# Kernel optimization log

Measured on AMD Instinct MI355X. Metric: run time of the kernel, lower is better.

Reference implementation:

```python
import jax, jax.numpy as jnp
import numpy as np

N = 100000
E = 1600000
G = 2048
D = 128
F_IN = 9
BN_EPS = 1e-5


def setup_inputs() -> dict:
    key = jax.random.key(0)
    ks = jax.random.split(key, 20)
    def glorot(k, shape):
        lim = float(np.sqrt(6.0 / (shape[0] + shape[1])))
        return jax.random.uniform(k, shape, jnp.float32, -lim, lim)
    inp = {
        'x': jax.random.normal(ks[0], (N, F_IN), jnp.float32),
        'edge_index': jax.random.randint(ks[1], (2, E), 0, N, jnp.int64),
        'batch_index': jnp.sort(jax.random.randint(ks[2], (N,), 0, G, jnp.int64)),
        'W0': glorot(ks[3], (F_IN, D)), 'b0': jnp.zeros((D,), jnp.float32),
        'W1': glorot(ks[4], (D, D)), 'b1': jnp.zeros((D,), jnp.float32),
        'W2': glorot(ks[5], (D, D)), 'b2': jnp.zeros((D,), jnp.float32),
        'W3': glorot(ks[6], (D, D)), 'b3': jnp.zeros((D,), jnp.float32),
        'g1': jnp.ones((D,), jnp.float32), 'be1': jnp.zeros((D,), jnp.float32),
        'g2': jnp.ones((D,), jnp.float32), 'be2': jnp.zeros((D,), jnp.float32),
        'g3': jnp.ones((D,), jnp.float32), 'be3': jnp.zeros((D,), jnp.float32),
        'Wout': glorot(ks[7], (D, 1)), 'bout': jnp.zeros((1,), jnp.float32),
    }
    return inp


def _gcn_conv(x, W, b, row, col, dinv):
    # PyG GCNConv: out = D^-1/2 (A+I) D^-1/2 (x W) + b
    lin = x @ W                                  # [N, D]
    coef = (dinv[row] * dinv[col])[:, None]      # [E, 1]
    agg = jax.ops.segment_sum(lin[row] * coef, col, num_segments=N)
    agg = agg + (dinv * dinv)[:, None] * lin     # self-loop term
    return agg + b


def _bn(x, gamma, beta):
    # BatchNorm1d training-mode: batch stats over node dim, biased variance
    m = jnp.mean(x, axis=0)
    v = jnp.var(x, axis=0)
    return (x - m) * jax.lax.rsqrt(v + BN_EPS) * gamma + beta


def reference(x, edge_index, batch_index, W0, b0, W1, b1, W2, b2, W3, b3,
              g1, be1, g2, be2, g3, be3, Wout, bout):
    row, col = edge_index[0], edge_index[1]
    # degrees with self-loops (all edge weights = 1)
    deg = jax.ops.segment_sum(jnp.ones((E,), x.dtype), col, num_segments=N) + 1.0
    dinv = jax.lax.rsqrt(deg)
    lrelu = lambda h: jax.nn.leaky_relu(h, negative_slope=0.01)

    h = _bn(lrelu(_gcn_conv(x, W0, b0, row, col, dinv)), g1, be1)
    h = _bn(lrelu(_gcn_conv(h, W1, b1, row, col, dinv)), g2, be2)
    h = _bn(lrelu(_gcn_conv(h, W2, b2, row, col, dinv)), g3, be3)
    h = lrelu(_gcn_conv(h, W3, b3, row, col, dinv))

    # global mean pool over graphs
    sums = jax.ops.segment_sum(h, batch_index, num_segments=G)
    cnts = jax.ops.segment_sum(jnp.ones((N,), x.dtype), batch_index, num_segments=G)
    pooled = sums / jnp.maximum(cnts, 1.0)[:, None]   # [G, D]
    return pooled @ Wout + bout                       # [G, 1]
```

## Files before the change

### kernel.cpp

```cpp
#include <hip/hip_runtime.h>


#define LRELU(z) ((z) > 0.f ? (z) : 0.01f * (z))

typedef __attribute__((ext_vector_type(8))) short short8;
typedef __attribute__((ext_vector_type(4))) float float4v;

__device__ inline unsigned bf16_rn(float a) {
  unsigned u = __float_as_uint(a);
  return (u + 0x7FFFu + ((u >> 16) & 1u)) >> 16;
}

__device__ inline unsigned pack_bf16x2(float a, float b) {
  return bf16_rn(a) | (bf16_rn(b) << 16);
}

__device__ inline float bf16f(unsigned short s) {
  return __uint_as_float(((unsigned)s) << 16);
}

__device__ inline float4 unpack_bf16x4(uint2 u) {
  float4 r;
  r.x = __uint_as_float(u.x << 16);
  r.y = __uint_as_float(u.x & 0xffff0000u);
  r.z = __uint_as_float(u.y << 16);
  r.w = __uint_as_float(u.y & 0xffff0000u);
  return r;
}

__device__ inline void accb(int4& d, unsigned v) {
  d.x += ((int)(v << 24)) >> 24;
  d.y += ((int)(v << 16)) >> 24;
  d.z += ((int)(v << 8)) >> 24;
  d.w += ((int)v) >> 24;
}

__global__ __launch_bounds__(256) void k_count(const int* __restrict__ ei,
                                               int* __restrict__ cnt,
                                               int* __restrict__ rank, int E) {
  int i = blockIdx.x * 256 + threadIdx.x;
  if (i < E) rank[i] = atomicAdd(&cnt[ei[E + i]], 1);
}

__global__ __launch_bounds__(256) void k_scan1(const int* __restrict__ cnt,
                                               int* __restrict__ incl,
                                               int* __restrict__ bsums,
                                               float* __restrict__ dinv, int N) {
  __shared__ int s[256];
  int tid = threadIdx.x;
  int idx = blockIdx.x * 256 + tid;
  int v = (idx < N) ? cnt[idx] : 0;
  if (idx < N) dinv[idx] = rsqrtf((float)(v + 1));
  s[tid] = v;
  __syncthreads();
  for (int off = 1; off < 256; off <<= 1) {
    int t = (tid >= off) ? s[tid - off] : 0;
    __syncthreads();
    s[tid] += t;
    __syncthreads();
  }
  if (idx < N) incl[idx] = s[tid];
  if (tid == 255) bsums[blockIdx.x] = s[255];
}

__global__ __launch_bounds__(512) void k_scan2(const int* __restrict__ bsums,
                                               int* __restrict__ bpref, int nb) {
  __shared__ int s[512];
  int tid = threadIdx.x;
  int v = (tid < nb) ? bsums[tid] : 0;
  s[tid] = v;
  __syncthreads();
  for (int off = 1; off < 512; off <<= 1) {
    int t = (tid >= off) ? s[tid - off] : 0;
    __syncthreads();
    s[tid] += t;
    __syncthreads();
  }
  bpref[tid] = s[tid] - v;
}

__global__ __launch_bounds__(256) void k_cntg(const int* __restrict__ batch,
                                              float* __restrict__ cntG,
                                              int N, int G) {
  int g = blockIdx.x * 256 + threadIdx.x;
  if (g >= G) return;
  int lo = 0, hi = N;
  while (lo < hi) { int mid = (lo + hi) >> 1; if (batch[mid] < g) lo = mid + 1; else hi = mid; }
  int a = lo;
  hi = N;
  while (lo < hi) { int mid = (lo + hi) >> 1; if (batch[mid] < g + 1) lo = mid + 1; else hi = mid; }
  cntG[g] = (float)(lo - a);
}

__global__ __launch_bounds__(256) void k_scan3_prep(
    const int* __restrict__ incl, const int* __restrict__ cnt,
    const int* __restrict__ bpref, int* __restrict__ offs,
    int2* __restrict__ meta, const float* __restrict__ x,
    const float* __restrict__ dinv, unsigned* __restrict__ u, int N) {
  int idx = blockIdx.x * 256 + threadIdx.x;
  if (idx >= N) return;
  int c = cnt[idx];
  int off = incl[idx] - c + bpref[blockIdx.x];
  offs[idx] = off;
  meta[idx] = make_int2(off, c);
  float dv = dinv[idx];
  const float* xr = x + (size_t)idx * 9;
  unsigned p0 = pack_bf16x2(xr[0] * dv, xr[1] * dv);
  unsigned p1 = pack_bf16x2(xr[2] * dv, xr[3] * dv);
  unsigned p2 = pack_bf16x2(xr[4] * dv, xr[5] * dv);
  unsigned p3 = pack_bf16x2(xr[6] * dv, xr[7] * dv);
  unsigned p4 = pack_bf16x2(xr[8] * dv, dv);
  uint2* u2 = (uint2*)u;
  u2[(size_t)idx * 3 + 0] = make_uint2(p0, p1);
  u2[(size_t)idx * 3 + 1] = make_uint2(p2, p3);
  u2[(size_t)idx * 3 + 2] = make_uint2(p4, 0u);
}

__global__ __launch_bounds__(256) void k_csr(const int* __restrict__ ei,
                                             const int* __restrict__ offs,
                                             const int* __restrict__ rank,
                                             int* __restrict__ rows, int E) {
  int i = blockIdx.x * 256 + threadIdx.x;
  if (i < E) {
    int c = ei[E + i];
    rows[offs[c] + rank[i]] = ei[i];
  }
}

__global__ __launch_bounds__(256) void k_spmm9(
    const unsigned short* __restrict__ u, const int2* __restrict__ meta,
    const int* __restrict__ rows, const float* __restrict__ dinv,
    float* __restrict__ ax, float2* __restrict__ dq, int N) {
  const int t = threadIdx.x;
  const int g = t >> 4;
  const int f = t & 15;
  const int v = blockIdx.x * 16 + g;
  if (v >= N) return;
  const int2 m = meta[v];
  const int st = m.x;
  const int dg = m.y;
  const float dv = dinv[v];
  const bool act = (f < 10);
  float a0 = (f < 9) ? bf16f(u[(unsigned)v * 12u + f]) : 0.f;
  float a1 = 0.f, a2 = 0.f, a3 = 0.f;
  int idx = 0;
  if (f < (dg < 16 ? dg : 16)) idx = rows[st + f];
  for (int b = 0; b < dg; b += 16) {
    int rem = dg - b;
    int mm = rem < 16 ? rem : 16;
    const int cur = idx;
    if (b + 16 < dg) idx = (f < rem - 16) ? rows[st + b + 16 + f] : 0;
    int e = 0;
    for (; e + 8 <= mm; e += 8) {
      int r0 = __shfl(cur, e + 0, 16), r1 = __shfl(cur, e + 1, 16);
      int r2 = __shfl(cur, e + 2, 16), r3 = __shfl(cur, e + 3, 16);
      int r4 = __shfl(cur, e + 4, 16), r5 = __shfl(cur, e + 5, 16);
      int r6 = __shfl(cur, e + 6, 16), r7 = __shfl(cur, e + 7, 16);
      float x0 = 0, x1 = 0, x2 = 0, x3 = 0, x4 = 0, x5 = 0, x6 = 0, x7 = 0;
      if (act) {
        x0 = bf16f(u[(unsigned)r0 * 12u + f]); x1 = bf16f(u[(unsigned)r1 * 12u + f]);
        x2 = bf16f(u[(unsigned)r2 * 12u + f]); x3 = bf16f(u[(unsigned)r3 * 12u + f]);
        x4 = bf16f(u[(unsigned)r4 * 12u + f]); x5 = bf16f(u[(unsigned)r5 * 12u + f]);
        x6 = bf16f(u[(unsigned)r6 * 12u + f]); x7 = bf16f(u[(unsigned)r7 * 12u + f]);
      }
      a0 += x0; a1 += x1; a2 += x2; a3 += x3;
      a0 += x4; a1 += x5; a2 += x6; a3 += x7;
    }
    for (; e + 4 <= mm; e += 4) {
      int r0 = __shfl(cur, e + 0, 16), r1 = __shfl(cur, e + 1, 16);
      int r2 = __shfl(cur, e + 2, 16), r3 = __shfl(cur, e + 3, 16);
      float x0 = 0, x1 = 0, x2 = 0, x3 = 0;
      if (act) {
        x0 = bf16f(u[(unsigned)r0 * 12u + f]); x1 = bf16f(u[(unsigned)r1 * 12u + f]);
        x2 = bf16f(u[(unsigned)r2 * 12u + f]); x3 = bf16f(u[(unsigned)r3 * 12u + f]);
      }
      a0 += x0; a1 += x1; a2 += x2; a3 += x3;
    }
    for (; e < mm; e++) {
      int r = __shfl(cur, e, 16);
      if (act) a0 += bf16f(u[(unsigned)r * 12u + f]);
    }
  }
  float sum = (a0 + a1) + (a2 + a3);
  if (f < 9) {
    ax[(unsigned)v * 12u + f] = sum * dv;
  } else if (f == 9) {
    dq[v] = make_float2(dv, dv * (dv + sum));
  }
}

__global__ __launch_bounds__(256) void k_gemm_in(
    const float* __restrict__ ax, const float* __restrict__ W0,
    const float* __restrict__ b0, unsigned short* __restrict__ Abuf,
    float* __restrict__ part, int N) {
  __shared__ float Wl[9 * 128];
  __shared__ float rs[128], rq[128];
  const int t = threadIdx.x;
  for (int i = t; i < 9 * 128; i += 256) Wl[i] = W0[i];
  if (t < 128) { rs[t] = 0.f; rq[t] = 0.f; }
  __syncthreads();
  const int col = t & 127;
  const int rsub = t >> 7;
  const int base = blockIdx.x * 16;
  const float bc = b0[col];
  float ls = 0.f, lq = 0.f;
  for (int it = 0; it < 8; it++) {
    int row = base + it * 2 + rsub;
    if (row < N) {
      const float* ar = ax + (size_t)row * 12;
      float acc = bc;
#pragma unroll
      for (int k = 0; k < 9; k++) acc += ar[k] * Wl[k * 128 + col];
      float a = LRELU(acc);
      Abuf[(size_t)row * 128 + col] = (unsigned short)bf16_rn(a);
      ls += a;
      lq += a * a;
    }
  }
  atomicAdd(&rs[col], ls);
  atomicAdd(&rq[col], lq);
  __syncthreads();
  if (t < 128) {
    float* pr = part + (size_t)blockIdx.x * 256;
    pr[t] = rs[t];
    pr[128 + t] = rq[t];
  }
}

__global__ __launch_bounds__(256) void k_redstats(const float* __restrict__ part,
                                                  float* __restrict__ stats,
                                                  int nrows) {
  const int t = threadIdx.x;
  float s = 0.f;
  for (int r = blockIdx.x; r < nrows; r += gridDim.x)
    s += part[(size_t)r * 256 + t];
  atomicAdd(&stats[t], s);
}

__global__ __launch_bounds__(256) void k_gemm_mfma(
    const unsigned short* __restrict__ Ab, const uint4* __restrict__ Wb,
    const float* __restrict__ dinv, unsigned short* __restrict__ Lb,
    unsigned* __restrict__ colmaxU, int N) {
  __shared__ uint4 Bl[2048];
  __shared__ unsigned short Dl[4 * 2048];
  __shared__ float dvs[64];
  __shared__ unsigned cmx[128];
  const int t = threadIdx.x;
  const int row0 = blockIdx.x * 64;
#pragma unroll
  for (int i = 0; i < 8; i++) Bl[t + i * 256] = Wb[t + i * 256];
  if (t < 128) cmx[t] = 0u;
  if (t < 64) {
    int r = row0 + t;
    dvs[t] = (r < N) ? dinv[r] : 0.f;
  }
  __syncthreads();
  const int w = t >> 6;
  const int lane = t & 63;
  const int m = lane & 15;
  const int quad = lane >> 4;
  const int rowA = min(row0 + w * 16 + m, N - 1);
  const uint4* Arow = (const uint4*)(Ab + (size_t)rowA * 128);
  uint4 a[4];
#pragma unroll
  for (int kt = 0; kt < 4; kt++) a[kt] = Arow[kt * 4 + quad];
  float4v acc[8];
#pragma unroll
  for (int nt = 0; nt < 8; nt++) acc[nt] = (float4v)0.0f;
#pragma unroll
  for (int nt = 0; nt < 8; nt++) {
#pragma unroll
    for (int kt = 0; kt < 4; kt++) {
      uint4 b = Bl[((kt * 8 + nt) * 4 + quad) * 16 + m];
      acc[nt] = __builtin_amdgcn_mfma_f32_16x16x32_bf16(
          *(short8*)&a[kt], *(short8*)&b, acc[nt], 0, 0, 0);
    }
  }
  unsigned short* Dw = Dl + w * 2048;
  float cm8[8];
#pragma unroll
  for (int nt = 0; nt < 8; nt++) cm8[nt] = 0.f;
#pragma unroll
  for (int r = 0; r < 4; r++) {
    float dv = dvs[w * 16 + quad * 4 + r];
#pragma unroll
    for (int nt = 0; nt < 8; nt++) {
      float fv = acc[nt][r] * dv;
      Dw[(quad * 4 + r) * 128 + nt * 16 + m] = (unsigned short)bf16_rn(fv);
      cm8[nt] = fmaxf(cm8[nt], fabsf(fv));
    }
  }
#pragma unroll
  for (int nt = 0; nt < 8; nt++)
    atomicMax(&cmx[nt * 16 + m], __float_as_uint(cm8[nt]));
  __syncthreads();
  const uint4* Dw4 = (const uint4*)Dw;
#pragma unroll
  for (int p = 0; p < 4; p++) {
    int row = row0 + w * 16 + p * 4 + (lane >> 4);
    if (row < N) {
      ((uint4*)(Lb + (size_t)row * 128))[lane & 15] = Dw4[p * 64 + lane];
    }
  }
  if (t < 128) atomicMax(&colmaxU[t], cmx[t]);
}

__global__ __launch_bounds__(256) void k_quant(
    const unsigned short* __restrict__ Lb, const unsigned* __restrict__ cmU,
    unsigned* __restrict__ L8, int N4) {
  __shared__ float invS[128];
  const int t = threadIdx.x;
  if (t < 128) {
    float cm = __uint_as_float(cmU[t]);
    invS[t] = cm > 0.f ? 127.f / cm : 0.f;
  }
  __syncthreads();
  int idx = blockIdx.x * 256 + t;
  if (idx >= N4) return;
  const int row = idx >> 2;
  const int seg = idx & 3;
  const uint2* src = (const uint2*)(Lb + (size_t)row * 128 + seg * 32);
  const float* inv = invS + seg * 32;
  unsigned d[8];
#pragma unroll
  for (int j = 0; j < 8; j++) {
    float4 f = unpack_bf16x4(src[j]);
    int q0 = __float2int_rn(f.x * inv[j * 4 + 0]);
    int q1 = __float2int_rn(f.y * inv[j * 4 + 1]);
    int q2 = __float2int_rn(f.z * inv[j * 4 + 2]);
    int q3 = __float2int_rn(f.w * inv[j * 4 + 3]);
    q0 = max(-127, min(127, q0));
    q1 = max(-127, min(127, q1));
    q2 = max(-127, min(127, q2));
    q3 = max(-127, min(127, q3));
    d[j] = (unsigned)(q0 & 255) | ((unsigned)(q1 & 255) << 8) |
           ((unsigned)(q2 & 255) << 16) | ((unsigned)(q3 & 255) << 24);
  }
  uint4* dst = (uint4*)((char*)L8 + (size_t)row * 128 + (size_t)seg * 32);
  dst[0] = make_uint4(d[0], d[1], d[2], d[3]);
  dst[1] = make_uint4(d[4], d[5], d[6], d[7]);
}

__device__ inline int4 gacci(const unsigned* __restrict__ L8d,
                             const int* __restrict__ rows,
                             int st, int dg, int idx, int q32) {
  int4 s0 = make_int4(0, 0, 0, 0), s1 = s0, s2 = s0, s3 = s0;
  for (int b = 0; b < dg; b += 32) {
    int rem = dg - b;
    int mm = rem < 32 ? rem : 32;
    const int cur = idx;
    if (b + 32 < dg) idx = (q32 < rem - 32) ? rows[st + b + 32 + q32] : 0;
    int e = 0;
    for (; e + 8 <= mm; e += 8) {
      int r0 = __shfl(cur, e + 0, 32), r1 = __shfl(cur, e + 1, 32);
      int r2 = __shfl(cur, e + 2, 32), r3 = __shfl(cur, e + 3, 32);
      int r4 = __shfl(cur, e + 4, 32), r5 = __shfl(cur, e + 5, 32);
      int r6 = __shfl(cur, e + 6, 32), r7 = __shfl(cur, e + 7, 32);
      unsigned w0 = L8d[((unsigned)r0 << 5) + q32];
      unsigned w1 = L8d[((unsigned)r1 << 5) + q32];
      unsigned w2 = L8d[((unsigned)r2 << 5) + q32];
      unsigned w3 = L8d[((unsigned)r3 << 5) + q32];
      unsigned w4 = L8d[((unsigned)r4 << 5) + q32];
      unsigned w5 = L8d[((unsigned)r5 << 5) + q32];
      unsigned w6 = L8d[((unsigned)r6 << 5) + q32];
      unsigned w7 = L8d[((unsigned)r7 << 5) + q32];
      accb(s0, w0); accb(s1, w1); accb(s2, w2); accb(s3, w3);
      accb(s0, w4); accb(s1, w5); accb(s2, w6); accb(s3, w7);
    }
    for (; e + 4 <= mm; e += 4) {
      int r0 = __shfl(cur, e + 0, 32), r1 = __shfl(cur, e + 1, 32);
      int r2 = __shfl(cur, e + 2, 32), r3 = __shfl(cur, e + 3, 32);
      unsigned w0 = L8d[((unsigned)r0 << 5) + q32];
      unsigned w1 = L8d[((unsigned)r1 << 5) + q32];
      unsigned w2 = L8d[((unsigned)r2 << 5) + q32];
      unsigned w3 = L8d[((unsigned)r3 << 5) + q32];
      accb(s0, w0); accb(s1, w1); accb(s2, w2); accb(s3, w3);
    }
    for (; e < mm; e++) {
      int r = __shfl(cur, e, 32);
      unsigned w0 = L8d[((unsigned)r << 5) + q32];
      accb(s0, w0);
    }
  }
  int4 acc;
  acc.x = (s0.x + s1.x) + (s2.x + s3.x);
  acc.y = (s0.y + s1.y) + (s2.y + s3.y);
  acc.z = (s0.z + s1.z) + (s2.z + s3.z);
  acc.w = (s0.w + s1.w) + (s2.w + s3.w);
  return acc;
}

template <int MODE>
__global__ __launch_bounds__(256) void k_spmm(
    const unsigned* __restrict__ Lb, const unsigned* __restrict__ L8d,
    const unsigned* __restrict__ cmU, const int2* __restrict__ meta,
    const int* __restrict__ rows, const float2* __restrict__ dq,
    const float* __restrict__ tw, const float* __restrict__ bias,
    unsigned short* __restrict__ Aout, float* __restrict__ part,
    const float* __restrict__ wout, const int* __restrict__ batch,
    float* __restrict__ pacc, int N) {
  const int t = threadIdx.x;
  const int g = t >> 5;
  const int q32 = t & 31;
  const uint2* __restrict__ L2p = (const uint2*)Lb;
  const float4 t4 = ((const float4*)tw)[q32];
  const float4 b4 = ((const float4*)bias)[q32];
  const float4 cm4 = ((const float4*)(const void*)cmU)[q32];
  const float ksc = 1.f / 127.f;
  const float4 s4 = make_float4(cm4.x * ksc, cm4.y * ksc, cm4.z * ksc, cm4.w * ksc);
  float4 wo4 = make_float4(0.f, 0.f, 0.f, 0.f);
  if (MODE == 1) wo4 = ((const float4*)wout)[q32];
  __shared__ float rs[128], rq[128];
  __shared__ float psum[16];
  __shared__ int pb[16];
  float4 ls = make_float4(0.f, 0.f, 0.f, 0.f), lq = ls;
  if (MODE == 0) {
    if (t < 128) { rs[t] = 0.f; rq[t] = 0.f; }
  } else {
    if (t < 16) pb[t] = -1;
  }
  __syncthreads();
  const int vb = blockIdx.x * 16 + g * 2;
  const bool ok0 = vb < N, ok1 = vb + 1 < N;
  const int v0 = ok0 ? vb : N - 1;
  const int v1 = ok1 ? vb + 1 : N - 1;
  const int2 m0 = meta[v0];
  const int2 m1 = meta[v1];
  const float2 dq0 = dq[v0];
  const float2 dq1 = dq[v1];
  uint2 self0 = L2p[((unsigned)v0 << 5) + q32];
  uint2 self1 = L2p[((unsigned)v1 << 5) + q32];
  int bt0 = 0, bt1 = 0;
  if (MODE == 1) { bt0 = batch[v0]; bt1 = batch[v1]; }
  int i0 = 0, i1 = 0;
  if (q32 < (m0.y < 32 ? m0.y : 32)) i0 = rows[m0.x + q32];
  if (q32 < (m1.y < 32 ? m1.y : 32)) i1 = rows[m1.x + q32];
  int4 ia0 = gacci(L8d, rows, m0.x, m0.y, i0, q32);
  int4 ia1 = gacci(L8d, rows, m1.x, m1.y, i1, q32);
  float4 sf0 = unpack_bf16x4(self0);
  float4 sf1 = unpack_bf16x4(self1);
  float4 acc0, acc1;
  acc0.x = sf0.x + (float)ia0.x * s4.x;
  acc0.y = sf0.y + (float)ia0.y * s4.y;
  acc0.z = sf0.z + (float)ia0.z * s4.z;
  acc0.w = sf0.w + (float)ia0.w * s4.w;
  acc1.x = sf1.x + (float)ia1.x * s4.x;
  acc1.y = sf1.y + (float)ia1.y * s4.y;
  acc1.z = sf1.z + (float)ia1.z * s4.z;
  acc1.w = sf1.w + (float)ia1.w * s4.w;
  float4 a0, a1;
  a0.x = LRELU(dq0.x * acc0.x + dq0.y * t4.x + b4.x);
  a0.y = LRELU(dq0.x * acc0.y + dq0.y * t4.y + b4.y);
  a0.z = LRELU(dq0.x * acc0.z + dq0.y * t4.z + b4.z);
  a0.w = LRELU(dq0.x * acc0.w + dq0.y * t4.w + b4.w);
  a1.x = LRELU(dq1.x * acc1.x + dq1.y * t4.x + b4.x);
  a1.y = LRELU(dq1.x * acc1.y + dq1.y * t4.y + b4.y);
  a1.z = LRELU(dq1.x * acc1.z + dq1.y * t4.z + b4.z);
  a1.w = LRELU(dq1.x * acc1.w + dq1.y * t4.w + b4.w);
  if (MODE == 0) {
    if (ok0) {
      uint2 p;
      p.x = pack_bf16x2(a0.x, a0.y);
      p.y = pack_bf16x2(a0.z, a0.w);
      ((uint2*)Aout)[((unsigned)v0 << 5) + q32] = p;
      ls.x += a0.x; ls.y += a0.y; ls.z += a0.z; ls.w += a0.w;
      lq.x += a0.x * a0.x; lq.y += a0.y * a0.y;
      lq.z += a0.z * a0.z; lq.w += a0.w * a0.w;
    }
    if (ok1) {
      uint2 p;
      p.x = pack_bf16x2(a1.x, a1.y);
      p.y = pack_bf16x2(a1.z, a1.w);
      ((uint2*)Aout)[((unsigned)v1 << 5) + q32] = p;
      ls.x += a1.x; ls.y += a1.y; ls.z += a1.z; ls.w += a1.w;
      lq.x += a1.x * a1.x; lq.y += a1.y * a1.y;
      lq.z += a1.z * a1.z; lq.w += a1.w * a1.w;
    }
    const int f0 = q32 * 4;
    atomicAdd(&rs[f0 + 0], ls.x); atomicAdd(&rs[f0 + 1], ls.y);
    atomicAdd(&rs[f0 + 2], ls.z); atomicAdd(&rs[f0 + 3], ls.w);
    atomicAdd(&rq[f0 + 0], lq.x); atomicAdd(&rq[f0 + 1], lq.y);
    atomicAdd(&rq[f0 + 2], lq.z); atomicAdd(&rq[f0 + 3], lq.w);
    __syncthreads();
    if (t < 128) {
      float* pr = part + (size_t)blockIdx.x * 256;
      pr[t] = rs[t];
      pr[128 + t] = rq[t];
    }
  } else {
    float sA = a0.x * wo4.x + a0.y * wo4.y + a0.z * wo4.z + a0.w * wo4.w;
    sA += __shfl_down(sA, 16, 32);
    sA += __shfl_down(sA, 8, 32);
    sA += __shfl_down(sA, 4, 32);
    sA += __shfl_down(sA, 2, 32);
    sA += __shfl_down(sA, 1, 32);
    float sB = a1.x * wo4.x + a1.y * wo4.y + a1.z * wo4.z + a1.w * wo4.w;
    sB += __shfl_down(sB, 16, 32);
    sB += __shfl_down(sB, 8, 32);
    sB += __shfl_down(sB, 4, 32);
    sB += __shfl_down(sB, 2, 32);
    sB += __shfl_down(sB, 1, 32);
    if (q32 == 0) {
      if (ok0) { psum[g * 2 + 0] = sA; pb[g * 2 + 0] = bt0; }
      if (ok1) { psum[g * 2 + 1] = sB; pb[g * 2 + 1] = bt1; }
    }
    __syncthreads();
    if (t < 16) {
      int b = pb[t];
      if (b >= 0 && (t == 0 || pb[t - 1] != b)) {
        float s = psum[t];
        for (int j = t + 1; j < 16 && pb[j] == b; j++) s += psum[j];
        atomicAdd(&pacc[b], s);
      }
    }
  }
}

__global__ __launch_bounds__(128) void k_fold(const float* __restrict__ stats,
                                              const float* __restrict__ g,
                                              const float* __restrict__ be,
                                              const float* __restrict__ W,
                                              unsigned short* __restrict__ Wb,
                                              float* __restrict__ tw, float invN) {
  const int j = threadIdx.x;
  const int i0 = blockIdx.x * 16;
  const int nt = j >> 4;
  const int n = j & 15;
  float acc = 0.f;
#pragma unroll
  for (int ii = 0; ii < 16; ii++) {
    int i = i0 + ii;
    float m = stats[i] * invN;
    float var = stats[128 + i] * invN - m * m;
    float si = g[i] * rsqrtf(var + 1e-5f);
    float ti = be[i] - m * si;
    float w = W[i * 128 + j];
    acc += ti * w;
    int kt = i >> 5, quad = (i >> 3) & 3, jj = i & 7;
    Wb[((((kt * 8 + nt) * 4 + quad) * 16 + n) << 3) + jj] =
        (unsigned short)bf16_rn(si * w);
  }
  atomicAdd(&tw[j], acc);
}

__global__ __launch_bounds__(256) void k_out(const float* __restrict__ pacc,
                                             const float* __restrict__ cntG,
                                             const float* __restrict__ bout,
                                             float* __restrict__ out, int G) {
  int i = blockIdx.x * 256 + threadIdx.x;
  if (i < G) out[i] = pacc[i] / fmaxf(cntG[i], 1.0f) + bout[0];
}

extern "C" void kernel_launch(void* const* d_in, const int* in_sizes, int n_in,
                              void* d_out, int out_size, void* d_ws, size_t ws_size,
                              hipStream_t stream) {
  const float* x    = (const float*)d_in[0];
  const int*   ei   = (const int*)d_in[1];
  const int*   batch= (const int*)d_in[2];
  const float* W0   = (const float*)d_in[3];
  const float* b0   = (const float*)d_in[4];
  const float* W1   = (const float*)d_in[5];
  const float* b1   = (const float*)d_in[6];
  const float* W2   = (const float*)d_in[7];
  const float* b2   = (const float*)d_in[8];
  const float* W3   = (const float*)d_in[9];
  const float* b3   = (const float*)d_in[10];
  const float* g1   = (const float*)d_in[11];
  const float* be1  = (const float*)d_in[12];
  const float* g2   = (const float*)d_in[13];
  const float* be2  = (const float*)d_in[14];
  const float* g3   = (const float*)d_in[15];
  const float* be3  = (const float*)d_in[16];
  const float* Wout = (const float*)d_in[17];
  const float* bout = (const float*)d_in[18];
  float* out = (float*)d_out;

  const int N = in_sizes[0] / 9;
  const int E = in_sizes[1] / 2;
  const int G = out_size;

  char* w = (char*)d_ws;
  auto alloc = [&](size_t bytes) -> void* {
    void* p = (void*)w;
    w += (bytes + 255) & ~(size_t)255;
    return p;
  };
  char* zbase = w;
  int*   cnt    = (int*)alloc((size_t)N * 4);
  float* pacc   = (float*)alloc((size_t)G * 4);
  float* stats  = (float*)alloc(3 * 256 * 4);
  float* tw3    = (float*)alloc(3 * 128 * 4);
  unsigned* cmU3 = (unsigned*)alloc(3 * 128 * 4);
  size_t zsize = (size_t)(w - zbase);
  int*   offs   = (int*)alloc((size_t)N * 4);
  int*   incl   = (int*)alloc((size_t)N * 4);
  int*   bsums  = (int*)alloc(512 * 4);
  int*   bpref  = (int*)alloc(512 * 4);
  float* dinv   = (float*)alloc((size_t)N * 4);
  float2* dq    = (float2*)alloc((size_t)N * 8);
  int2*  meta   = (int2*)alloc((size_t)N * 8);
  float* cntG   = (float*)alloc((size_t)G * 4);
  int*   rank   = (int*)alloc((size_t)E * 4);
  int*   rows   = (int*)alloc((size_t)E * 4);
  unsigned short* Wb = (unsigned short*)alloc(128 * 128 * 2);
  unsigned* u   = (unsigned*)alloc((size_t)N * 12 * 2);
  float* ax     = (float*)alloc((size_t)N * 12 * 4);
  unsigned* Lb  = (unsigned*)alloc((size_t)N * 128 * 2);
  unsigned* L8  = (unsigned*)alloc((size_t)N * 128);
  unsigned short* Abuf = (unsigned short*)alloc((size_t)N * 128 * 2);
  const int sb  = (N + 15) / 16;
  float* part   = (float*)alloc((size_t)sb * 256 * 4);

  hipMemsetAsync(zbase, 0, zsize, stream);

  const int eb  = (E + 255) / 256;
  const int nbN = (N + 255) / 256;
  const int mb  = (N + 63) / 64;
  const int qb  = (N * 4 + 255) / 256;
  const float invN = 1.0f / (float)N;
  float* twA = tw3;
  float* twB = tw3 + 128;
  float* twC = tw3 + 256;
  unsigned* cmA = cmU3;
  unsigned* cmB = cmU3 + 128;
  unsigned* cmC = cmU3 + 256;

  k_count<<<eb, 256, 0, stream>>>(ei, cnt, rank, E);
  k_scan1<<<nbN, 256, 0, stream>>>(cnt, incl, bsums, dinv, N);
  k_scan2<<<1, 512, 0, stream>>>(bsums, bpref, nbN);
  k_scan3_prep<<<nbN, 256, 0, stream>>>(incl, cnt, bpref, offs, meta, x, dinv, u, N);
  k_csr<<<eb, 256, 0, stream>>>(ei, offs, rank, rows, E);
  k_cntg<<<(G + 255) / 256, 256, 0, stream>>>(batch, cntG, N, G);

  k_spmm9<<<sb, 256, 0, stream>>>((const unsigned short*)u, meta, rows,
                                  dinv, ax, dq, N);
  k_gemm_in<<<sb, 256, 0, stream>>>(ax, W0, b0, Abuf, part, N);
  k_redstats<<<64, 256, 0, stream>>>(part, stats, sb);
  k_fold<<<8, 128, 0, stream>>>(stats, g1, be1, W1, Wb, twA, invN);
  k_gemm_mfma<<<mb, 256, 0, stream>>>(Abuf, (const uint4*)Wb, dinv,
                                      (unsigned short*)Lb, cmA, N);
  k_quant<<<qb, 256, 0, stream>>>((const unsigned short*)Lb, cmA, L8, N * 4);
  k_spmm<0><<<sb, 256, 0, stream>>>(Lb, L8, cmA, meta, rows, dq, twA, b1,
                                    Abuf, part, nullptr, nullptr, nullptr, N);
  k_redstats<<<64, 256, 0, stream>>>(part, stats + 256, sb);
  k_fold<<<8, 128, 0, stream>>>(stats + 256, g2, be2, W2, Wb, twB, invN);
  k_gemm_mfma<<<mb, 256, 0, stream>>>(Abuf, (const uint4*)Wb, dinv,
                                      (unsigned short*)Lb, cmB, N);
  k_quant<<<qb, 256, 0, stream>>>((const unsigned short*)Lb, cmB, L8, N * 4);
  k_spmm<0><<<sb, 256, 0, stream>>>(Lb, L8, cmB, meta, rows, dq, twB, b2,
                                    Abuf, part, nullptr, nullptr, nullptr, N);
  k_redstats<<<64, 256, 0, stream>>>(part, stats + 512, sb);
  k_fold<<<8, 128, 0, stream>>>(stats + 512, g3, be3, W3, Wb, twC, invN);
  k_gemm_mfma<<<mb, 256, 0, stream>>>(Abuf, (const uint4*)Wb, dinv,
                                      (unsigned short*)Lb, cmC, N);
  k_quant<<<qb, 256, 0, stream>>>((const unsigned short*)Lb, cmC, L8, N * 4);
  k_spmm<1><<<sb, 256, 0, stream>>>(Lb, L8, cmC, meta, rows, dq, twC, b3,
                                    nullptr, nullptr, Wout, batch, pacc, N);
  k_out<<<(G + 255) / 256, 256, 0, stream>>>(pacc, cntG, bout, out, G);
}
```

Before: 724.6 us.

## Pad input rows to 32 bytes, vectorize loads, fold graph counts into output

Several small changes at once. The bf16 packed input feature rows are padded from 24 to 32 bytes so that prep writes two uint4 stores and the gather in spmm9 reads aligned rows. The first GEMM reads its 9 input features as three float4 loads instead of scalar loads. The per-graph count kernel is merged into the final output kernel, which removes one launch, and the stats reduction runs with twice as many blocks. The padding adds some memory footprint and gather bandwidth in exchange for alignment.

```diff
diff --git a/kernel.cpp b/kernel.cpp
--- a/kernel.cpp
+++ b/kernel.cpp
@@ -77,19 +77,6 @@
     __syncthreads();
   }
   bpref[tid] = s[tid] - v;
-}
-
-__global__ __launch_bounds__(256) void k_cntg(const int* __restrict__ batch,
-                                              float* __restrict__ cntG,
-                                              int N, int G) {
-  int g = blockIdx.x * 256 + threadIdx.x;
-  if (g >= G) return;
-  int lo = 0, hi = N;
-  while (lo < hi) { int mid = (lo + hi) >> 1; if (batch[mid] < g) lo = mid + 1; else hi = mid; }
-  int a = lo;
-  hi = N;
-  while (lo < hi) { int mid = (lo + hi) >> 1; if (batch[mid] < g + 1) lo = mid + 1; else hi = mid; }
-  cntG[g] = (float)(lo - a);
 }
 
 __global__ __launch_bounds__(256) void k_scan3_prep(
@@ -110,10 +97,9 @@
   unsigned p2 = pack_bf16x2(xr[4] * dv, xr[5] * dv);
   unsigned p3 = pack_bf16x2(xr[6] * dv, xr[7] * dv);
   unsigned p4 = pack_bf16x2(xr[8] * dv, dv);
-  uint2* u2 = (uint2*)u;
-  u2[(size_t)idx * 3 + 0] = make_uint2(p0, p1);
-  u2[(size_t)idx * 3 + 1] = make_uint2(p2, p3);
-  u2[(size_t)idx * 3 + 2] = make_uint2(p4, 0u);
+  uint4* u4 = (uint4*)u;
+  u4[(size_t)idx * 2 + 0] = make_uint4(p0, p1, p2, p3);
+  u4[(size_t)idx * 2 + 1] = make_uint4(p4, 0u, 0u, 0u);
 }
 
 __global__ __launch_bounds__(256) void k_csr(const int* __restrict__ ei,
@@ -141,7 +127,7 @@
   const int dg = m.y;
   const float dv = dinv[v];
   const bool act = (f < 10);
-  float a0 = (f < 9) ? bf16f(u[(unsigned)v * 12u + f]) : 0.f;
+  float a0 = (f < 9) ? bf16f(u[(unsigned)v * 16u + f]) : 0.f;
   float a1 = 0.f, a2 = 0.f, a3 = 0.f;
   int idx = 0;
   if (f < (dg < 16 ? dg : 16)) idx = rows[st + f];
@@ -158,10 +144,10 @@
       int r6 = __shfl(cur, e + 6, 16), r7 = __shfl(cur, e + 7, 16);
       float x0 = 0, x1 = 0, x2 = 0, x3 = 0, x4 = 0, x5 = 0, x6 = 0, x7 = 0;
       if (act) {
-        x0 = bf16f(u[(unsigned)r0 * 12u + f]); x1 = bf16f(u[(unsigned)r1 * 12u + f]);
-        x2 = bf16f(u[(unsigned)r2 * 12u + f]); x3 = bf16f(u[(unsigned)r3 * 12u + f]);
-        x4 = bf16f(u[(unsigned)r4 * 12u + f]); x5 = bf16f(u[(unsigned)r5 * 12u + f]);
-        x6 = bf16f(u[(unsigned)r6 * 12u + f]); x7 = bf16f(u[(unsigned)r7 * 12u + f]);
+        x0 = bf16f(u[(unsigned)r0 * 16u + f]); x1 = bf16f(u[(unsigned)r1 * 16u + f]);
+        x2 = bf16f(u[(unsigned)r2 * 16u + f]); x3 = bf16f(u[(unsigned)r3 * 16u + f]);
+        x4 = bf16f(u[(unsigned)r4 * 16u + f]); x5 = bf16f(u[(unsigned)r5 * 16u + f]);
+        x6 = bf16f(u[(unsigned)r6 * 16u + f]); x7 = bf16f(u[(unsigned)r7 * 16u + f]);
       }
       a0 += x0; a1 += x1; a2 += x2; a3 += x3;
       a0 += x4; a1 += x5; a2 += x6; a3 += x7;
@@ -171,14 +157,14 @@
       int r2 = __shfl(cur, e + 2, 16), r3 = __shfl(cur, e + 3, 16);
       float x0 = 0, x1 = 0, x2 = 0, x3 = 0;
       if (act) {
-        x0 = bf16f(u[(unsigned)r0 * 12u + f]); x1 = bf16f(u[(unsigned)r1 * 12u + f]);
-        x2 = bf16f(u[(unsigned)r2 * 12u + f]); x3 = bf16f(u[(unsigned)r3 * 12u + f]);
+        x0 = bf16f(u[(unsigned)r0 * 16u + f]); x1 = bf16f(u[(unsigned)r1 * 16u + f]);
+        x2 = bf16f(u[(unsigned)r2 * 16u + f]); x3 = bf16f(u[(unsigned)r3 * 16u + f]);
       }
       a0 += x0; a1 += x1; a2 += x2; a3 += x3;
     }
     for (; e < mm; e++) {
       int r = __shfl(cur, e, 16);
-      if (act) a0 += bf16f(u[(unsigned)r * 12u + f]);
+      if (act) a0 += bf16f(u[(unsigned)r * 16u + f]);
     }
   }
   float sum = (a0 + a1) + (a2 + a3);
@@ -207,10 +193,18 @@
   for (int it = 0; it < 8; it++) {
     int row = base + it * 2 + rsub;
     if (row < N) {
-      const float* ar = ax + (size_t)row * 12;
+      const float4* ar4 = (const float4*)(ax + (size_t)row * 12);
+      float4 v0 = ar4[0], v1 = ar4[1], v2 = ar4[2];
       float acc = bc;
-#pragma unroll
-      for (int k = 0; k < 9; k++) acc += ar[k] * Wl[k * 128 + col];
+      acc += v0.x * Wl[0 * 128 + col];
+      acc += v0.y * Wl[1 * 128 + col];
+      acc += v0.z * Wl[2 * 128 + col];
+      acc += v0.w * Wl[3 * 128 + col];
+      acc += v1.x * Wl[4 * 128 + col];
+      acc += v1.y * Wl[5 * 128 + col];
+      acc += v1.z * Wl[6 * 128 + col];
+      acc += v1.w * Wl[7 * 128 + col];
+      acc += v2.x * Wl[8 * 128 + col];
       float a = LRELU(acc);
       Abuf[(size_t)row * 128 + col] = (unsigned short)bf16_rn(a);
       ls += a;
@@ -544,11 +538,19 @@
 }
 
 __global__ __launch_bounds__(256) void k_out(const float* __restrict__ pacc,
-                                             const float* __restrict__ cntG,
+                                             const int* __restrict__ batch,
                                              const float* __restrict__ bout,
-                                             float* __restrict__ out, int G) {
-  int i = blockIdx.x * 256 + threadIdx.x;
-  if (i < G) out[i] = pacc[i] / fmaxf(cntG[i], 1.0f) + bout[0];
+                                             float* __restrict__ out,
+                                             int N, int G) {
+  int g = blockIdx.x * 256 + threadIdx.x;
+  if (g >= G) return;
+  int lo = 0, hi = N;
+  while (lo < hi) { int mid = (lo + hi) >> 1; if (batch[mid] < g) lo = mid + 1; else hi = mid; }
+  int a = lo;
+  hi = N;
+  while (lo < hi) { int mid = (lo + hi) >> 1; if (batch[mid] < g + 1) lo = mid + 1; else hi = mid; }
+  float cnt = (float)(lo - a);
+  out[g] = pacc[g] / fmaxf(cnt, 1.0f) + bout[0];
 }
 
 extern "C" void kernel_launch(void* const* d_in, const int* in_sizes, int n_in,
@@ -599,11 +601,10 @@
   float* dinv   = (float*)alloc((size_t)N * 4);
   float2* dq    = (float2*)alloc((size_t)N * 8);
   int2*  meta   = (int2*)alloc((size_t)N * 8);
-  float* cntG   = (float*)alloc((size_t)G * 4);
   int*   rank   = (int*)alloc((size_t)E * 4);
   int*   rows   = (int*)alloc((size_t)E * 4);
   unsigned short* Wb = (unsigned short*)alloc(128 * 128 * 2);
-  unsigned* u   = (unsigned*)alloc((size_t)N * 12 * 2);
+  unsigned* u   = (unsigned*)alloc((size_t)N * 16 * 2);
   float* ax     = (float*)alloc((size_t)N * 12 * 4);
   unsigned* Lb  = (unsigned*)alloc((size_t)N * 128 * 2);
   unsigned* L8  = (unsigned*)alloc((size_t)N * 128);
@@ -630,31 +631,30 @@
   k_scan2<<<1, 512, 0, stream>>>(bsums, bpref, nbN);
   k_scan3_prep<<<nbN, 256, 0, stream>>>(incl, cnt, bpref, offs, meta, x, dinv, u, N);
   k_csr<<<eb, 256, 0, stream>>>(ei, offs, rank, rows, E);
-  k_cntg<<<(G + 255) / 256, 256, 0, stream>>>(batch, cntG, N, G);
 
   k_spmm9<<<sb, 256, 0, stream>>>((const unsigned short*)u, meta, rows,
                                   dinv, ax, dq, N);
   k_gemm_in<<<sb, 256, 0, stream>>>(ax, W0, b0, Abuf, part, N);
-  k_redstats<<<64, 256, 0, stream>>>(part, stats, sb);
+  k_redstats<<<128, 256, 0, stream>>>(part, stats, sb);
   k_fold<<<8, 128, 0, stream>>>(stats, g1, be1, W1, Wb, twA, invN);
   k_gemm_mfma<<<mb, 256, 0, stream>>>(Abuf, (const uint4*)Wb, dinv,
                                       (unsigned short*)Lb, cmA, N);
   k_quant<<<qb, 256, 0, stream>>>((const unsigned short*)Lb, cmA, L8, N * 4);
   k_spmm<0><<<sb, 256, 0, stream>>>(Lb, L8, cmA, meta, rows, dq, twA, b1,
                                     Abuf, part, nullptr, nullptr, nullptr, N);
-  k_redstats<<<64, 256, 0, stream>>>(part, stats + 256, sb);
+  k_redstats<<<128, 256, 0, stream>>>(part, stats + 256, sb);
   k_fold<<<8, 128, 0, stream>>>(stats + 256, g2, be2, W2, Wb, twB, invN);
   k_gemm_mfma<<<mb, 256, 0, stream>>>(Abuf, (const uint4*)Wb, dinv,
                                       (unsigned short*)Lb, cmB, N);
   k_quant<<<qb, 256, 0, stream>>>((const unsigned short*)Lb, cmB, L8, N * 4);
   k_spmm<0><<<sb, 256, 0, stream>>>(Lb, L8, cmB, meta, rows, dq, twB, b2,
                                     Abuf, part, nullptr, nullptr, nullptr, N);
-  k_redstats<<<64, 256, 0, stream>>>(part, stats + 512, sb);
+  k_redstats<<<128, 256, 0, stream>>>(part, stats + 512, sb);
   k_fold<<<8, 128, 0, stream>>>(stats + 512, g3, be3, W3, Wb, twC, invN);
   k_gemm_mfma<<<mb, 256, 0, stream>>>(Abuf, (const uint4*)Wb, dinv,
                                       (unsigned short*)Lb, cmC, N);
   k_quant<<<qb, 256, 0, stream>>>((const unsigned short*)Lb, cmC, L8, N * 4);
   k_spmm<1><<<sb, 256, 0, stream>>>(Lb, L8, cmC, meta, rows, dq, twC, b3,
                                     nullptr, nullptr, Wout, batch, pacc, N);
-  k_out<<<(G + 255) / 256, 256, 0, stream>>>(pacc, cntG, bout, out, G);
-}
+  k_out<<<(G + 255) / 256, 256, 0, stream>>>(pacc, batch, bout, out, N, G);
+}
```

Measured after the change: 683.5 us, median of 2. -5.7%, faster.
